# Optimization experiments

Hardware: AMD Instinct MI355X
Metric: run time of the kernel (lower is better)

## Reference

```python
import jax, jax.numpy as jnp
import numpy as np

NUM_BUCKETS = 320
MAX_DISTANCE = 800


def _layer_norm(x, w, b, eps=1e-5):
    x32 = x.astype(jnp.float32)
    mu = x32.mean(-1, keepdims=True)
    var = x32.var(-1, keepdims=True)
    return ((x32 - mu) / jnp.sqrt(var + eps) * w + b).astype(x.dtype)


def _rel_pos_bucket(rel):
    half = NUM_BUCKETS // 2            # 160
    st = half // 2                     # 80 (small threshold)
    sign = (rel >= 0).astype(jnp.int32)
    ab = jnp.abs(rel)
    is_small = ab < st
    log_ratio = jnp.log(jnp.clip(ab.astype(jnp.float32), 1.0) / st) / np.float32(np.log(MAX_DISTANCE / st))
    log_pos = st + (log_ratio * (half - st)).astype(jnp.int32)  # trunc toward zero like .long()
    log_pos = jnp.minimum(log_pos, half - 1)
    bucket = jnp.where(is_small, ab, log_pos) + sign * half
    return jnp.clip(bucket, 0, NUM_BUCKETS - 1)


def setup_inputs() -> dict:
    key = jax.random.key(0)
    B, T, C, H, FF = 2, 2048, 768, 12, 3072
    D = C // H
    ks = jax.random.split(key, 16)
    s = 0.02
    return {
        "x": jax.random.normal(ks[0], (B, T, C), jnp.float32),
        "ln1_w": jnp.ones((C,), jnp.float32),
        "ln1_b": jnp.zeros((C,), jnp.float32),
        "wq": jax.random.normal(ks[1], (C, C), jnp.float32) * s,
        "bq": jnp.zeros((C,), jnp.float32),
        "wk": jax.random.normal(ks[2], (C, C), jnp.float32) * s,
        "bk": jnp.zeros((C,), jnp.float32),
        "wv": jax.random.normal(ks[3], (C, C), jnp.float32) * s,
        "bv": jnp.zeros((C,), jnp.float32),
        "wo": jax.random.normal(ks[4], (C, C), jnp.float32) * s,
        "bo": jnp.zeros((C,), jnp.float32),
        "ln2_w": jnp.ones((C,), jnp.float32),
        "ln2_b": jnp.zeros((C,), jnp.float32),
        "w1": jax.random.normal(ks[5], (FF, C), jnp.float32) * s,
        "b1": jnp.zeros((FF,), jnp.float32),
        "w2": jax.random.normal(ks[6], (C, FF), jnp.float32) * s,
        "b2": jnp.zeros((C,), jnp.float32),
        "rel_embed": jax.random.normal(ks[7], (NUM_BUCKETS, H), jnp.float32),
        "gate_ur_w": jax.random.normal(ks[8], (H, D), jnp.float32) * 0.01,
        "gate_i_w": jax.random.normal(ks[9], (H, D), jnp.float32) * 0.01,
        "rel_scale": jnp.ones((H,), jnp.float32),
    }


def reference(x, ln1_w, ln1_b, wq, bq, wk, bk, wv, bv, wo, bo,
              ln2_w, ln2_b, w1, b1, w2, b2, rel_embed, gate_ur_w, gate_i_w, rel_scale):
    B, T, C = x.shape
    H = rel_embed.shape[1]
    D = C // H

    residual = x
    h = _layer_norm(x, ln1_w, ln1_b)
    q = (h @ wq.T + bq).reshape(B, T, H, D).transpose(0, 2, 1, 3)  # [B,H,T,D]
    k = (h @ wk.T + bk).reshape(B, T, H, D).transpose(0, 2, 1, 3)
    v = (h @ wv.T + bv).reshape(B, T, H, D).transpose(0, 2, 1, 3)

    attn = jnp.einsum('bhqd,bhkd->bhqk', q, k) * (D ** -0.5)

    # gated relative position bias
    pos = jnp.arange(T)
    rel = pos[None, :] - pos[:, None]                 # [T,T]
    buckets = _rel_pos_bucket(rel)                    # [T,T]
    pe = rel_embed[buckets]                           # [T,T,H]
    pe = jnp.transpose(pe, (2, 0, 1))[None]           # [1,H,T,T]
    g_in = q.mean(axis=2).transpose(0, 2, 1).mean(axis=-1)   # [B,D]
    gate_r = jax.nn.sigmoid(g_in @ gate_ur_w.T)       # [B,H]
    gate_u = jax.nn.sigmoid(g_in @ gate_i_w.T)        # [B,H]
    gate = 1.0 + (gate_u * rel_scale[None, :] * gate_r)[:, :, None, None]
    bias = pe * gate                                  # [B,H,T,T]

    attn = jax.nn.softmax(attn + bias, axis=-1)
    out = jnp.einsum('bhqk,bhkd->bhqd', attn, v).transpose(0, 2, 1, 3).reshape(B, T, C)
    x = residual + out @ wo.T + bo

    residual = x
    h = _layer_norm(x, ln2_w, ln2_b)
    h = jax.nn.gelu(h @ w1.T + b1, approximate=False) @ w2.T + b2
    return residual + h
```

## Files before the change

kernel.cpp:

```cpp
#include <hip/hip_runtime.h>
#include <hip/hip_bf16.h>


#define Tn 2048
#define Cn 768
#define Hn 12
#define Dn 64
#define FFn 3072
#define Mn 4096
#define QKVS 2304
#define LQK 1536

typedef __attribute__((ext_vector_type(8))) short bfrag;
typedef __attribute__((ext_vector_type(8))) unsigned short us8;
typedef __attribute__((ext_vector_type(4))) float f32x4;

#define GLDS(gptr, lptr) __builtin_amdgcn_global_load_lds( \
    (const __attribute__((address_space(1))) void*)(gptr), \
    (__attribute__((address_space(3))) void*)(lptr), 16, 0, 0)

__device__ __forceinline__ unsigned short f2bu(float f){
  __hip_bfloat16 h = __float2bfloat16(f);
  return *(unsigned short*)&h;
}
__device__ __forceinline__ float bu2f(unsigned short u){
  union { unsigned int i; float f; } v; v.i = ((unsigned int)u) << 16; return v.f;
}
__device__ __forceinline__ us8 pack8(float4 a, float4 b){
  us8 c;
  c[0]=f2bu(a.x); c[1]=f2bu(a.y); c[2]=f2bu(a.z); c[3]=f2bu(a.w);
  c[4]=f2bu(b.x); c[5]=f2bu(b.y); c[6]=f2bu(b.z); c[7]=f2bu(b.w);
  return c;
}
__device__ __forceinline__ float fexp2(float x){ return __builtin_amdgcn_exp2f(x); }

__device__ __forceinline__ float block_reduce_sum(float v, float* sred){
  #pragma unroll
  for (int off = 32; off > 0; off >>= 1) v += __shfl_down(v, off, 64);
  __syncthreads();
  if ((threadIdx.x & 63) == 0) sred[threadIdx.x >> 6] = v;
  __syncthreads();
  return sred[0] + sred[1] + sred[2] + sred[3];
}

__global__ __launch_bounds__(256) void cast_all_kernel(
    const float* __restrict__ wq, const float* __restrict__ wk,
    const float* __restrict__ wv, const float* __restrict__ wo,
    const float* __restrict__ w1, const float* __restrict__ w2,
    const float* __restrict__ bq, const float* __restrict__ bk,
    const float* __restrict__ bv, const float* __restrict__ rel_embed,
    unsigned short* __restrict__ Wqkv, unsigned short* __restrict__ Wob,
    unsigned short* __restrict__ W1b, unsigned short* __restrict__ W2b,
    float* __restrict__ bias_rel, float* __restrict__ bqkv)
{
  const int blk = blockIdx.x;
  if (blk >= 3472){
    const int i = (blk - 3472) * 256 + threadIdx.x;
    bqkv[i] = (i < Cn) ? bq[i] : (i < 2 * Cn) ? bk[i - Cn] : bv[i - 2 * Cn];
    return;
  }
  if (blk >= 3456){
    const int idx = (blk - 3456) * 256 + threadIdx.x;
    if (idx >= 4095) return;
    const int rel = idx - 2047;
    const int ab = rel < 0 ? -rel : rel;
    int bucket;
    if (ab < 80){
      bucket = ab;
    } else {
      const float lr = logf((float)ab * (1.0f / 80.0f)) * (1.0f / 2.3025851f);
      int lp = 80 + (int)(lr * 80.0f);
      bucket = lp < 159 ? lp : 159;
    }
    if (rel >= 0) bucket += 160;
    #pragma unroll
    for (int h = 0; h < Hn; h++)
      bias_rel[h * 4095 + idx] = rel_embed[bucket * Hn + h] * 1.44269504089f;
    return;
  }
  const float* src; unsigned short* dst; int i;
  if (blk < 288)      { src = wq; dst = Wqkv;               i = blk * 256 + threadIdx.x; }
  else if (blk < 576) { src = wk; dst = Wqkv + Cn * Cn;     i = (blk - 288) * 256 + threadIdx.x; }
  else if (blk < 864) { src = wv; dst = Wqkv + 2 * Cn * Cn; i = (blk - 576) * 256 + threadIdx.x; }
  else if (blk < 1152){ src = wo; dst = Wob;                i = (blk - 864) * 256 + threadIdx.x; }
  else if (blk < 2304){ src = w1; dst = W1b;                i = (blk - 1152) * 256 + threadIdx.x; }
  else                { src = w2; dst = W2b;                i = (blk - 2304) * 256 + threadIdx.x; }
  const float4 a = ((const float4*)src)[i * 2];
  const float4 b = ((const float4*)src)[i * 2 + 1];
  *(us8*)&dst[i * 8] = pack8(a, b);
}

__global__ __launch_bounds__(256) void ln_kernel(const float* __restrict__ xin,
    const float* __restrict__ w, const float* __restrict__ bsh,
    unsigned short* __restrict__ out)
{
  __shared__ float xs[Cn];
  __shared__ float sred[4];
  const size_t base = (size_t)blockIdx.x * Cn;
  float s = 0.f;
  for (int c = threadIdx.x; c < Cn; c += 256){
    float v = xin[base + c];
    xs[c] = v; s += v;
  }
  const float mean = block_reduce_sum(s, sred) * (1.f / Cn);
  float s2 = 0.f;
  for (int c = threadIdx.x; c < Cn; c += 256){
    float d = xs[c] - mean; s2 += d * d;
  }
  const float var = block_reduce_sum(s2, sred) * (1.f / Cn);
  const float rstd = rsqrtf(var + 1e-5f);
  for (int c = threadIdx.x; c < Cn; c += 256)
    out[base + c] = f2bu((xs[c] - mean) * rstd * w[c] + bsh[c]);
}

template<int EPI, bool TRANSV>
__global__ __launch_bounds__(256) void gemm_mfma_kernel(
    const unsigned short* __restrict__ A, const unsigned short* __restrict__ Bw,
    const float* __restrict__ bias, unsigned short* __restrict__ vt,
    void* __restrict__ Cout, int M, int N, int K, int ldo)
{
  __shared__ __align__(16) unsigned short As[2 * 128 * 32];
  __shared__ __align__(16) unsigned short Bs[2 * 128 * 32];
  const int tid = threadIdx.x;
  const int lane = tid & 63, w = tid >> 6;
  const int nl = lane & 15, quad = lane >> 4;
  const int wm = w >> 1, wn = w & 1;
  const int id = blockIdx.x;
  const int bm = ((id & 7) * 4 + ((id >> 3) & 3)) * 128;
  const int bn = (id >> 5) * 128;
  const int l4 = lane >> 2, lk = (lane & 3) * 8;

  f32x4 acc[4][4];
  #pragma unroll
  for (int i = 0; i < 4; i++)
    #pragma unroll
    for (int j = 0; j < 4; j++) acc[i][j] = (f32x4){0.f, 0.f, 0.f, 0.f};

  const int c0 = w, c1 = w + 4;
  const unsigned short* A0 = A + (size_t)(bm + c0 * 16 + l4) * K + lk;
  const unsigned short* A1 = A + (size_t)(bm + c1 * 16 + l4) * K + lk;
  const unsigned short* B0 = Bw + (size_t)(bn + c0 * 16 + l4) * K + lk;
  const unsigned short* B1 = Bw + (size_t)(bn + c1 * 16 + l4) * K + lk;

  for (int k0 = 0; k0 < K; k0 += 64){
    __syncthreads();
    GLDS(A0 + k0,      &As[c0 * 512]);
    GLDS(A0 + k0 + 32, &As[4096 + c0 * 512]);
    GLDS(A1 + k0,      &As[c1 * 512]);
    GLDS(A1 + k0 + 32, &As[4096 + c1 * 512]);
    GLDS(B0 + k0,      &Bs[c0 * 512]);
    GLDS(B0 + k0 + 32, &Bs[4096 + c0 * 512]);
    GLDS(B1 + k0,      &Bs[c1 * 512]);
    GLDS(B1 + k0 + 32, &Bs[4096 + c1 * 512]);
    __syncthreads();
    #pragma unroll
    for (int p = 0; p < 2; p++){
      bfrag Af[4], Bf[4];
      #pragma unroll
      for (int mt = 0; mt < 4; mt++)
        Af[mt] = *(const bfrag*)&As[p * 4096 + (wm * 64 + mt * 16 + nl) * 32 + quad * 8];
      #pragma unroll
      for (int nt = 0; nt < 4; nt++)
        Bf[nt] = *(const bfrag*)&Bs[p * 4096 + (wn * 64 + nt * 16 + nl) * 32 + quad * 8];
      #pragma unroll
      for (int mt = 0; mt < 4; mt++)
        #pragma unroll
        for (int nt = 0; nt < 4; nt++)
          acc[mt][nt] = __builtin_amdgcn_mfma_f32_16x16x32_bf16(Af[mt], Bf[nt], acc[mt][nt], 0, 0, 0);
    }
  }

  if (TRANSV && bn >= 1536){
    #pragma unroll
    for (int nt = 0; nt < 4; nt++){
      const int col = bn + wn * 64 + nt * 16 + nl;
      const float bv_ = bias[col];
      const int vcol = col - 1536;
      #pragma unroll
      for (int mt = 0; mt < 4; mt++){
        const int row0 = bm + wm * 64 + mt * 16 + quad * 4;
        unsigned short pk[4];
        #pragma unroll
        for (int r = 0; r < 4; r++) pk[r] = f2bu(acc[mt][nt][r] + bv_);
        *(uint2*)&vt[(size_t)vcol * Mn + row0] = *(uint2*)pk;
      }
    }
    return;
  }
  #pragma unroll
  for (int nt = 0; nt < 4; nt++){
    const int col = bn + wn * 64 + nt * 16 + nl;
    const float bv_ = bias[col];
    #pragma unroll
    for (int mt = 0; mt < 4; mt++){
      const int row0 = bm + wm * 64 + mt * 16 + quad * 4;
      #pragma unroll
      for (int r = 0; r < 4; r++){
        const size_t idx = (size_t)(row0 + r) * ldo + col;
        const float v = acc[mt][nt][r] + bv_;
        if (EPI == 2){
          ((unsigned short*)Cout)[idx] = f2bu(0.5f * v * (1.f + erff(v * 0.70710678118f)));
        } else {
          ((unsigned short*)Cout)[idx] = f2bu(v);
        }
      }
    }
  }
}

__global__ __launch_bounds__(256) void gemm_t64_kernel(
    const unsigned short* __restrict__ A, const unsigned short* __restrict__ Bw,
    const float* __restrict__ bias, const float* __restrict__ res,
    float* __restrict__ Cout, int M, int N, int K)
{
  __shared__ __align__(16) unsigned short As[2 * 64 * 32];
  __shared__ __align__(16) unsigned short Bs[2 * 64 * 32];
  const int tid = threadIdx.x;
  const int lane = tid & 63, w = tid >> 6;
  const int nl = lane & 15, quad = lane >> 4;
  const int id = blockIdx.x;
  const int bm = ((id & 7) * 8 + ((id >> 3) & 7)) * 64;
  const int bn = (id >> 6) * 64;
  const int l2 = lane >> 2, l3 = (lane & 3) * 8;

  f32x4 acc[4];
  #pragma unroll
  for (int j = 0; j < 4; j++) acc[j] = (f32x4){0.f, 0.f, 0.f, 0.f};

  const unsigned short* A0 = A + (size_t)(bm + w * 16 + l2) * K + l3;
  const unsigned short* B0 = Bw + (size_t)(bn + w * 16 + l2) * K + l3;

  for (int k0 = 0; k0 < K; k0 += 64){
    __syncthreads();
    GLDS(A0 + k0,      &As[w * 512]);
    GLDS(A0 + k0 + 32, &As[2048 + w * 512]);
    GLDS(B0 + k0,      &Bs[w * 512]);
    GLDS(B0 + k0 + 32, &Bs[2048 + w * 512]);
    __syncthreads();
    const bfrag Af0 = *(const bfrag*)&As[(w * 16 + nl) * 32 + quad * 8];
    const bfrag Af1 = *(const bfrag*)&As[2048 + (w * 16 + nl) * 32 + quad * 8];
    bfrag Bf0[4], Bf1[4];
    #pragma unroll
    for (int nt = 0; nt < 4; nt++){
      Bf0[nt] = *(const bfrag*)&Bs[(nt * 16 + nl) * 32 + quad * 8];
      Bf1[nt] = *(const bfrag*)&Bs[2048 + (nt * 16 + nl) * 32 + quad * 8];
    }
    #pragma unroll
    for (int nt = 0; nt < 4; nt++){
      acc[nt] = __builtin_amdgcn_mfma_f32_16x16x32_bf16(Af0, Bf0[nt], acc[nt], 0, 0, 0);
      acc[nt] = __builtin_amdgcn_mfma_f32_16x16x32_bf16(Af1, Bf1[nt], acc[nt], 0, 0, 0);
    }
  }

  const int row0 = bm + w * 16 + quad * 4;
  #pragma unroll
  for (int nt = 0; nt < 4; nt++){
    const int col = bn + nt * 16 + nl;
    const float bv_ = bias[col];
    #pragma unroll
    for (int r = 0; r < 4; r++){
      const size_t idx = (size_t)(row0 + r) * N + col;
      Cout[idx] = acc[nt][r] + bv_ + res[idx];
    }
  }
}

__global__ __launch_bounds__(256) void qmean_part_kernel(
    const unsigned short* __restrict__ QKVqk, float* __restrict__ qpart)
{
  __shared__ float ps[Cn];
  const int b = blockIdx.y, t0 = blockIdx.x * 128;
  const int tid = threadIdx.x;
  float a0 = 0.f, a1 = 0.f, a2 = 0.f;
  for (int r = 0; r < 128; r++){
    const size_t base = (size_t)(b * Tn + t0 + r) * LQK;
    a0 += bu2f(QKVqk[base + tid]);
    a1 += bu2f(QKVqk[base + tid + 256]);
    a2 += bu2f(QKVqk[base + tid + 512]);
  }
  ps[tid] = a0; ps[tid + 256] = a1; ps[tid + 512] = a2;
  __syncthreads();
  if (tid < Dn){
    float s = 0.f;
    #pragma unroll
    for (int hh = 0; hh < Hn; hh++) s += ps[hh * Dn + tid];
    qpart[(b * 16 + blockIdx.x) * Dn + tid] = s;
  }
}

__global__ __launch_bounds__(64) void gate_kernel(const float* __restrict__ qpart,
    const float* __restrict__ gur, const float* __restrict__ gi,
    const float* __restrict__ rsc, float* __restrict__ gate)
{
  const int b = blockIdx.x / Hn, h = blockIdx.x % Hn;
  const int d = threadIdx.x;
  float s = 0.f;
  #pragma unroll
  for (int blk = 0; blk < 16; blk++) s += qpart[(b * 16 + blk) * Dn + d];
  const float g = s * (1.f / (Hn * Tn));
  float vr = g * gur[h * Dn + d];
  float vu = g * gi[h * Dn + d];
  #pragma unroll
  for (int off = 32; off > 0; off >>= 1){
    vr += __shfl_down(vr, off, 64);
    vu += __shfl_down(vu, off, 64);
  }
  if (d == 0){
    const float gr = 1.f / (1.f + __expf(-vr));
    const float gu = 1.f / (1.f + __expf(-vu));
    gate[blockIdx.x] = 1.f + gu * rsc[h] * gr;
  }
}

__global__ __launch_bounds__(256) void attn_mfma_kernel(
    const unsigned short* __restrict__ QKVqk, const unsigned short* __restrict__ VT,
    const float* __restrict__ bias_rel, const float* __restrict__ gate,
    unsigned short* __restrict__ O)
{
  __shared__ __align__(16) char smem[52224];
  unsigned short* Qs = (unsigned short*)smem;
  float* bias_blk    = (float*)smem;
  unsigned short* KsP = (unsigned short*)(smem + 9216);
  unsigned short* VtP = (unsigned short*)(smem + 25600);
  unsigned short* Ptq = (unsigned short*)(smem + 41984);
  float* lsh         = (float*)(smem + 51200);

  const int qbase = blockIdx.x * 64;
  const int h = blockIdx.y, b = blockIdx.z;
  const int tid = threadIdx.x;
  const float g = gate[b * Hn + h];
  const float* brow = bias_rel + h * 4095 + 1984 - qbase;
  const unsigned short* Q = QKVqk;
  const unsigned short* K = QKVqk + Cn;

  const int lane = tid & 63, w = tid >> 6;
  const int nl = lane & 15, quad = lane >> 4;
  const int l2 = lane >> 2, l3 = (lane & 3) * 8;

  const unsigned short* kg0 = K + (size_t)(b * Tn + w * 16 + l2) * LQK + h * Dn + l3;
  const unsigned short* vg0 = VT + (size_t)(h * Dn + w * 16 + l2) * Mn + (size_t)b * Tn + l3;

  GLDS(kg0,      KsP + w * 512);
  GLDS(kg0 + 32, KsP + 2048 + w * 512);
  GLDS(vg0,      VtP + w * 512);
  GLDS(vg0 + 32, VtP + 2048 + w * 512);

  {
    const int row = tid >> 2, cg = (tid & 3) * 16;
    const us8* qp = (const us8*)(Q + (size_t)(b * Tn + qbase + row) * LQK + h * Dn + cg);
    *(us8*)&Qs[row * 72 + cg]     = qp[0];
    *(us8*)&Qs[row * 72 + cg + 8] = qp[1];
  }
  __syncthreads();

  bfrag Qb[4][2];
  #pragma unroll
  for (int mt = 0; mt < 4; mt++){
    Qb[mt][0] = *(const bfrag*)&Qs[(mt * 16 + nl) * 72 + quad * 8];
    Qb[mt][1] = *(const bfrag*)&Qs[(mt * 16 + nl) * 72 + 32 + quad * 8];
  }
  __syncthreads();
  for (int j = tid; j < 2111; j += 256) bias_blk[j] = brow[j] * g;

  const int wq = w & 1, wd = w >> 1;
  f32x4 Oa[2][2];
  #pragma unroll
  for (int a = 0; a < 2; a++)
    #pragma unroll
    for (int d0 = 0; d0 < 2; d0++) Oa[a][d0] = (f32x4){0.f, 0.f, 0.f, 0.f};
  float l_part[4] = {0.f, 0.f, 0.f, 0.f};

  for (int kt = 0; kt < 32; kt++){
    const int kbase = kt * 64;
    const int cur = (kt & 1) * 4096;
    const int nxt = 4096 - cur;
    __syncthreads();
    if (kt < 31){
      const unsigned short* kg = kg0 + (size_t)(kbase + 64) * LQK;
      const unsigned short* vg = vg0 + kbase + 64;
      GLDS(kg,      KsP + nxt + w * 512);
      GLDS(kg + 32, KsP + nxt + 2048 + w * 512);
      GLDS(vg,      VtP + nxt + w * 512);
      GLDS(vg + 32, VtP + nxt + 2048 + w * 512);
    }

    const bfrag Ka0 = *(const bfrag*)&KsP[cur + (w * 16 + nl) * 32 + quad * 8];
    const bfrag Ka1 = *(const bfrag*)&KsP[cur + 2048 + (w * 16 + nl) * 32 + quad * 8];
    const int bofs = kbase + w * 16 + quad * 4 + 63 - nl;
    #pragma unroll
    for (int mt = 0; mt < 4; mt++){
      f32x4 z = (f32x4){0.f, 0.f, 0.f, 0.f};
      z = __builtin_amdgcn_mfma_f32_16x16x32_bf16(Ka0, Qb[mt][0], z, 0, 0, 0);
      z = __builtin_amdgcn_mfma_f32_16x16x32_bf16(Ka1, Qb[mt][1], z, 0, 0, 0);
      unsigned short pk[4];
      #pragma unroll
      for (int r = 0; r < 4; r++){
        const float p = fexp2(z[r] * 0.18033688f + bias_blk[bofs - mt * 16 + r]);
        l_part[mt] += p;
        pk[r] = f2bu(p);
      }
      *(uint2*)&Ptq[(mt * 16 + nl) * 72 + w * 16 + quad * 4] = *(uint2*)pk;
    }
    __syncthreads();

    bfrag Vf[2][2], Pf[2][2];
    #pragma unroll
    for (int d0 = 0; d0 < 2; d0++){
      const int dt = wd * 2 + d0;
      Vf[d0][0] = *(const bfrag*)&VtP[cur + (dt * 16 + nl) * 32 + quad * 8];
      Vf[d0][1] = *(const bfrag*)&VtP[cur + 2048 + (dt * 16 + nl) * 32 + quad * 8];
    }
    #pragma unroll
    for (int a = 0; a < 2; a++){
      const int qt = wq * 2 + a;
      Pf[a][0] = *(const bfrag*)&Ptq[(qt * 16 + nl) * 72 + quad * 8];
      Pf[a][1] = *(const bfrag*)&Ptq[(qt * 16 + nl) * 72 + 32 + quad * 8];
    }
    #pragma unroll
    for (int a = 0; a < 2; a++)
      #pragma unroll
      for (int d0 = 0; d0 < 2; d0++){
        Oa[a][d0] = __builtin_amdgcn_mfma_f32_16x16x32_bf16(Vf[d0][0], Pf[a][0], Oa[a][d0], 0, 0, 0);
        Oa[a][d0] = __builtin_amdgcn_mfma_f32_16x16x32_bf16(Vf[d0][1], Pf[a][1], Oa[a][d0], 0, 0, 0);
      }
  }

  #pragma unroll
  for (int mt = 0; mt < 4; mt++){
    float l = l_part[mt];
    l += __shfl_xor(l, 16, 64);
    l += __shfl_xor(l, 32, 64);
    if (quad == 0) lsh[w * 64 + mt * 16 + nl] = l;
  }
  __syncthreads();
  #pragma unroll
  for (int a = 0; a < 2; a++){
    const int q = (wq * 2 + a) * 16 + nl;
    const float linv = 1.f / (lsh[q] + lsh[64 + q] + lsh[128 + q] + lsh[192 + q]);
    unsigned short* orow = O + (size_t)(b * Tn + qbase + q) * Cn + h * Dn;
    #pragma unroll
    for (int d0 = 0; d0 < 2; d0++){
      unsigned short pk[4];
      #pragma unroll
      for (int r = 0; r < 4; r++) pk[r] = f2bu(Oa[a][d0][r] * linv);
      *(uint2*)&orow[(wd * 2 + d0) * 16 + quad * 4] = *(uint2*)pk;
    }
  }
}

extern "C" void kernel_launch(void* const* d_in, const int* in_sizes, int n_in,
                              void* d_out, int out_size, void* d_ws, size_t ws_size,
                              hipStream_t stream)
{
  const float* x     = (const float*)d_in[0];
  const float* ln1_w = (const float*)d_in[1];
  const float* ln1_b = (const float*)d_in[2];
  const float* wq    = (const float*)d_in[3];
  const float* bq    = (const float*)d_in[4];
  const float* wk    = (const float*)d_in[5];
  const float* bk    = (const float*)d_in[6];
  const float* wv    = (const float*)d_in[7];
  const float* bv    = (const float*)d_in[8];
  const float* wo    = (const float*)d_in[9];
  const float* bo    = (const float*)d_in[10];
  const float* ln2_w = (const float*)d_in[11];
  const float* ln2_b = (const float*)d_in[12];
  const float* w1    = (const float*)d_in[13];
  const float* b1    = (const float*)d_in[14];
  const float* w2    = (const float*)d_in[15];
  const float* b2    = (const float*)d_in[16];
  const float* rel_embed = (const float*)d_in[17];
  const float* gur   = (const float*)d_in[18];
  const float* gi    = (const float*)d_in[19];
  const float* rsc   = (const float*)d_in[20];

  char* ws = (char*)d_ws;
  unsigned short* QKVqk = (unsigned short*)(ws);
  unsigned short* VT    = (unsigned short*)(ws + 12582912);
  unsigned short* Ob    = (unsigned short*)(ws + 18874368);
  float*          X2    = (float*)(ws + 25165824);
  unsigned short* Hb    = (unsigned short*)(ws + 37748736);
  unsigned short* Wqkv  = (unsigned short*)(ws + 44040192);
  unsigned short* Wob   = (unsigned short*)(ws + 47579136);
  unsigned short* W1b   = (unsigned short*)(ws + 48758784);
  unsigned short* W2b   = (unsigned short*)(ws + 53477376);
  float*          bqkv  = (float*)(ws + 58195968);
  float*          bias_rel = (float*)(ws + 58205184);
  float*          qpart = (float*)(ws + 58401744);
  float*          gate  = (float*)(ws + 58409936);
  unsigned short* Fb    = (unsigned short*)(ws);

  cast_all_kernel<<<3481, 256, 0, stream>>>(wq, wk, wv, wo, w1, w2, bq, bk, bv,
                                            rel_embed, Wqkv, Wob, W1b, W2b,
                                            bias_rel, bqkv);
  ln_kernel<<<Mn, 256, 0, stream>>>(x, ln1_w, ln1_b, Hb);
  gemm_mfma_kernel<0, true><<<(QKVS / 128) * (Mn / 128), 256, 0, stream>>>(
      Hb, Wqkv, bqkv, VT, QKVqk, Mn, QKVS, Cn, LQK);
  qmean_part_kernel<<<dim3(16, 2), 256, 0, stream>>>(QKVqk, qpart);
  gate_kernel<<<2 * Hn, 64, 0, stream>>>(qpart, gur, gi, rsc, gate);
  attn_mfma_kernel<<<dim3(Tn / 64, Hn, 2), 256, 0, stream>>>(QKVqk, VT, bias_rel, gate, Ob);
  gemm_t64_kernel<<<(Cn / 64) * (Mn / 64), 256, 0, stream>>>(
      Ob, Wob, bo, x, X2, Mn, Cn, Cn);
  ln_kernel<<<Mn, 256, 0, stream>>>(X2, ln2_w, ln2_b, Hb);
  gemm_mfma_kernel<2, false><<<(FFn / 128) * (Mn / 128), 256, 0, stream>>>(
      Hb, W1b, b1, nullptr, Fb, Mn, FFn, Cn, FFn);
  gemm_t64_kernel<<<(Cn / 64) * (Mn / 64), 256, 0, stream>>>(
      Fb, W2b, b2, X2, (float*)d_out, Mn, Cn, FFn);
}
```

Baseline: 332.2 us.

## Double-buffer LDS tiles in both MFMA GEMM kernels to overlap loads with compute

```diff
diff --git a/kernel.cpp b/kernel.cpp
--- a/kernel.cpp
+++ b/kernel.cpp
@@ -119,8 +119,8 @@
     const float* __restrict__ bias, unsigned short* __restrict__ vt,
     void* __restrict__ Cout, int M, int N, int K, int ldo)
 {
-  __shared__ __align__(16) unsigned short As[2 * 128 * 32];
-  __shared__ __align__(16) unsigned short Bs[2 * 128 * 32];
+  __shared__ __align__(16) unsigned short As[2][128 * 32];
+  __shared__ __align__(16) unsigned short Bs[2][128 * 32];
   const int tid = threadIdx.x;
   const int lane = tid & 63, w = tid >> 6;
   const int nl = lane & 15, quad = lane >> 4;
@@ -142,32 +142,32 @@
   const unsigned short* B0 = Bw + (size_t)(bn + c0 * 16 + l4) * K + lk;
   const unsigned short* B1 = Bw + (size_t)(bn + c1 * 16 + l4) * K + lk;
 
-  for (int k0 = 0; k0 < K; k0 += 64){
+  GLDS(A0, &As[0][c0 * 512]); GLDS(A1, &As[0][c1 * 512]);
+  GLDS(B0, &Bs[0][c0 * 512]); GLDS(B1, &Bs[0][c1 * 512]);
+
+  const int NIT = K >> 5;
+  for (int t = 0; t < NIT; t++){
+    const int cur = t & 1;
     __syncthreads();
-    GLDS(A0 + k0,      &As[c0 * 512]);
-    GLDS(A0 + k0 + 32, &As[4096 + c0 * 512]);
-    GLDS(A1 + k0,      &As[c1 * 512]);
-    GLDS(A1 + k0 + 32, &As[4096 + c1 * 512]);
-    GLDS(B0 + k0,      &Bs[c0 * 512]);
-    GLDS(B0 + k0 + 32, &Bs[4096 + c0 * 512]);
-    GLDS(B1 + k0,      &Bs[c1 * 512]);
-    GLDS(B1 + k0 + 32, &Bs[4096 + c1 * 512]);
-    __syncthreads();
-    #pragma unroll
-    for (int p = 0; p < 2; p++){
-      bfrag Af[4], Bf[4];
-      #pragma unroll
-      for (int mt = 0; mt < 4; mt++)
-        Af[mt] = *(const bfrag*)&As[p * 4096 + (wm * 64 + mt * 16 + nl) * 32 + quad * 8];
+    if (t + 1 < NIT){
+      const int k0 = (t + 1) << 5;
+      GLDS(A0 + k0, &As[cur ^ 1][c0 * 512]);
+      GLDS(A1 + k0, &As[cur ^ 1][c1 * 512]);
+      GLDS(B0 + k0, &Bs[cur ^ 1][c0 * 512]);
+      GLDS(B1 + k0, &Bs[cur ^ 1][c1 * 512]);
+    }
+    bfrag Af[4], Bf[4];
+    #pragma unroll
+    for (int mt = 0; mt < 4; mt++)
+      Af[mt] = *(const bfrag*)&As[cur][(wm * 64 + mt * 16 + nl) * 32 + quad * 8];
+    #pragma unroll
+    for (int nt = 0; nt < 4; nt++)
+      Bf[nt] = *(const bfrag*)&Bs[cur][(wn * 64 + nt * 16 + nl) * 32 + quad * 8];
+    #pragma unroll
+    for (int mt = 0; mt < 4; mt++)
       #pragma unroll
       for (int nt = 0; nt < 4; nt++)
-        Bf[nt] = *(const bfrag*)&Bs[p * 4096 + (wn * 64 + nt * 16 + nl) * 32 + quad * 8];
-      #pragma unroll
-      for (int mt = 0; mt < 4; mt++)
-        #pragma unroll
-        for (int nt = 0; nt < 4; nt++)
-          acc[mt][nt] = __builtin_amdgcn_mfma_f32_16x16x32_bf16(Af[mt], Bf[nt], acc[mt][nt], 0, 0, 0);
-    }
+        acc[mt][nt] = __builtin_amdgcn_mfma_f32_16x16x32_bf16(Af[mt], Bf[nt], acc[mt][nt], 0, 0, 0);
   }
 
   if (TRANSV && bn >= 1536){
@@ -213,8 +213,8 @@
     const float* __restrict__ bias, const float* __restrict__ res,
     float* __restrict__ Cout, int M, int N, int K)
 {
-  __shared__ __align__(16) unsigned short As[2 * 64 * 32];
-  __shared__ __align__(16) unsigned short Bs[2 * 64 * 32];
+  __shared__ __align__(16) unsigned short As[2][2 * 64 * 32];
+  __shared__ __align__(16) unsigned short Bs[2][2 * 64 * 32];
   const int tid = threadIdx.x;
   const int lane = tid & 63, w = tid >> 6;
   const int nl = lane & 15, quad = lane >> 4;
@@ -230,20 +230,29 @@
   const unsigned short* A0 = A + (size_t)(bm + w * 16 + l2) * K + l3;
   const unsigned short* B0 = Bw + (size_t)(bn + w * 16 + l2) * K + l3;
 
-  for (int k0 = 0; k0 < K; k0 += 64){
+  GLDS(A0,      &As[0][w * 512]);
+  GLDS(A0 + 32, &As[0][2048 + w * 512]);
+  GLDS(B0,      &Bs[0][w * 512]);
+  GLDS(B0 + 32, &Bs[0][2048 + w * 512]);
+
+  const int NIT = K >> 6;
+  for (int t = 0; t < NIT; t++){
+    const int cur = t & 1;
     __syncthreads();
-    GLDS(A0 + k0,      &As[w * 512]);
-    GLDS(A0 + k0 + 32, &As[2048 + w * 512]);
-    GLDS(B0 + k0,      &Bs[w * 512]);
-    GLDS(B0 + k0 + 32, &Bs[2048 + w * 512]);
-    __syncthreads();
-    const bfrag Af0 = *(const bfrag*)&As[(w * 16 + nl) * 32 + quad * 8];
-    const bfrag Af1 = *(const bfrag*)&As[2048 + (w * 16 + nl) * 32 + quad * 8];
+    if (t + 1 < NIT){
+      const int k0 = (t + 1) << 6;
+      GLDS(A0 + k0,      &As[cur ^ 1][w * 512]);
+      GLDS(A0 + k0 + 32, &As[cur ^ 1][2048 + w * 512]);
+      GLDS(B0 + k0,      &Bs[cur ^ 1][w * 512]);
+      GLDS(B0 + k0 + 32, &Bs[cur ^ 1][2048 + w * 512]);
+    }
+    const bfrag Af0 = *(const bfrag*)&As[cur][(w * 16 + nl) * 32 + quad * 8];
+    const bfrag Af1 = *(const bfrag*)&As[cur][2048 + (w * 16 + nl) * 32 + quad * 8];
     bfrag Bf0[4], Bf1[4];
     #pragma unroll
     for (int nt = 0; nt < 4; nt++){
-      Bf0[nt] = *(const bfrag*)&Bs[(nt * 16 + nl) * 32 + quad * 8];
-      Bf1[nt] = *(const bfrag*)&Bs[2048 + (nt * 16 + nl) * 32 + quad * 8];
+      Bf0[nt] = *(const bfrag*)&Bs[cur][(nt * 16 + nl) * 32 + quad * 8];
+      Bf1[nt] = *(const bfrag*)&Bs[cur][2048 + (nt * 16 + nl) * 32 + quad * 8];
     }
     #pragma unroll
     for (int nt = 0; nt < 4; nt++){
```

Measured after the change: 318.6 us. 4.1% less time.
